# Kernel optimization log

Measured on AMD Instinct MI355X. Metric: run time of the kernel, lower is better.

Reference implementation:

```python
import jax, jax.numpy as jnp
import numpy as np

B = 4096
INPUT_SIZE = 256
OUT_WINDOW = 10
C = 16
OUTPUT_SIZE = 2  # real/imag pair
WIN = INPUT_SIZE - OUT_WINDOW + 1  # 247
BN_EPS = 1e-5


def setup_inputs() -> dict:
    key = jax.random.key(0)
    ks = jax.random.split(key, 7)
    return {
        "x": jax.random.normal(ks[0], (B, INPUT_SIZE, C, 2), dtype=jnp.float32),
        "W_in_real": jax.random.normal(ks[1], (C, WIN), dtype=jnp.float32),
        "W_in_imag": jax.random.normal(ks[2], (C, WIN), dtype=jnp.float32),
        "W_nl": jax.random.normal(ks[3], (C, OUTPUT_SIZE, 2 * (C - 1)), dtype=jnp.float32) * 0.1,
        "W_coeff": jax.random.normal(ks[4], (OUTPUT_SIZE, OUTPUT_SIZE), dtype=jnp.float32),
        "W_out_real": jax.random.normal(ks[5], (C, OUT_WINDOW), dtype=jnp.float32),
        "W_out_imag": jax.random.normal(ks[6], (C, OUT_WINDOW), dtype=jnp.float32),
        "bn_gamma": jnp.ones((C,), jnp.float32),
        "bn_beta": jnp.zeros((C,), jnp.float32),
    }


def _depthwise_filter(x_bcn, w_ck):
    # per-channel valid cross-correlation: out[b,c,w] = sum_k x[b,c,w+k] * w_ck[c,k]
    kern = w_ck[:, None, :]  # (O=C, I/groups=1, K)
    return jax.lax.conv_general_dilated(
        x_bcn, kern, window_strides=(1,), padding="VALID",
        dimension_numbers=("NCH", "OIH", "NCH"), feature_group_count=C)


def reference(x, W_in_real, W_in_imag, W_nl, W_coeff, W_out_real, W_out_imag, bn_gamma, bn_beta):
    # x: [B, N, C, 2]
    x_real = jnp.transpose(x[..., 0], (0, 2, 1))  # [B, C, N]
    x_imag = jnp.transpose(x[..., 1], (0, 2, 1))
    # unfold + per-channel FIR filter == depthwise valid correlation -> [B, W, C]
    f_r = jnp.transpose(_depthwise_filter(x_real, W_in_real), (0, 2, 1))
    f_i = jnp.transpose(_depthwise_filter(x_imag, W_in_imag), (0, 2, 1))
    # cubic amplitude nonlinearity
    amp = f_r * f_r + f_i * f_i
    f_r = amp * f_r
    f_i = amp * f_i
    # masked cross-channel gather (all channels except self), static indices
    nbr = np.stack([np.delete(np.arange(C), c) for c in range(C)])  # [C, C-1]
    nonlin_in = jnp.concatenate([f_r[:, :, nbr], f_i[:, :, nbr]], axis=-1)  # [B, W, C, 2(C-1)]
    # per-channel mixing then shared coeff mix
    nonlin_out = jnp.einsum("bwcf,cof->bwco", nonlin_in, W_nl)   # [B, W, C, 2]
    coeff_out = jnp.einsum("bwco,po->bwcp", nonlin_out, W_coeff)  # [B, W, C, 2]
    # per-channel output FIR over the out_window axis
    out_r = jnp.einsum("bwc,cw->bc", coeff_out[..., 0], W_out_real)
    out_i = jnp.einsum("bwc,cw->bc", coeff_out[..., 1], W_out_imag)
    out = jnp.stack([out_r, out_i], axis=-1)  # [B, C, 2]
    # BatchNorm1d over channel axis C (training mode, biased batch stats)
    mu = jnp.mean(out, axis=(0, 2))
    var = jnp.mean(jnp.square(out - mu[None, :, None]), axis=(0, 2))
    scale = (bn_gamma * jax.lax.rsqrt(var + BN_EPS))[None, :, None]
    return (out - mu[None, :, None]) * scale + bn_beta[None, :, None]
```

## Files before the change

### kernel.cpp

```cpp
#include <hip/hip_runtime.h>

#define BTOT 4096
#define G 4
#define NC 16
#define WIN 247
#define NBLK (BTOT / G)

typedef float v2f __attribute__((ext_vector_type(2)));

#define F2IDX(m, c) ((m) * 16 + (c) + ((m) >> 6) * 8)
#define WTSZ 4272

__global__ __launch_bounds__(256, 4) void k_main(
    const float* __restrict__ x,
    const float* __restrict__ Wr, const float* __restrict__ Wi,
    const float* __restrict__ Wnl, const float* __restrict__ Wc,
    const float* __restrict__ Wor, const float* __restrict__ Woi,
    float* __restrict__ out, float2* __restrict__ p2)
{
    __shared__ v2f WT[WTSZ];
    __shared__ float Mlds[4 * 16 * 17];
    __shared__ float WoS[2 * 160];
    __shared__ float WcS[4];

    const int tid  = threadIdx.x;
    const int lane = tid & 63;
    const int wv   = tid >> 6;
    const int jj   = lane >> 4;
    const int c    = lane & 15;
    const int b0   = blockIdx.x * G;

    for (int idx = tid; idx < 265 * 16; idx += 256) {
        int m = idx >> 4, cc = idx & 15;
        int t = m - 9;
        v2f v = (v2f)(0.f);
        if (t >= 0 && t < WIN) { v.x = Wr[cc * WIN + t]; v.y = Wi[cc * WIN + t]; }
        WT[F2IDX(m, cc)] = v;
    }
    for (int idx = tid; idx < 1024; idx += 256) {
        int m  = idx >> 8;
        int cc = (idx >> 4) & 15;
        int j  = idx & 15;
        float v = 0.f;
        if (j != cc) {
            int jp = j - (j > cc);
            v = Wnl[cc * 60 + (m >> 1) * 30 + (m & 1) * 15 + jp];
        }
        Mlds[m * 272 + cc * 17 + j] = v;
    }
    if (tid < 160) { WoS[tid] = Wor[tid]; WoS[160 + tid] = Woi[tid]; }
    if (tid < 4) WcS[tid] = Wc[tid];
    __syncthreads();

    const v2f* xq = (const v2f*)x + (size_t)(b0 + wv) * 4096 + lane;

    v2f acc[10];
    v2f win[14];
    v2f xr[8];
    #pragma unroll
    for (int w = 0; w < 10; ++w) acc[w] = (v2f)(0.f);

    #pragma unroll
    for (int d = 0; d < 14; ++d) win[d] = WT[F2IDX(d + jj, c)];
    #pragma unroll
    for (int j = 0; j < 8; ++j) xr[j] = xq[j * 64];

    #pragma unroll
    for (int i = 0; i < 64; ++i) {
        v2f xv = xr[i & 7];
        if (i < 56) xr[i & 7] = xq[(i + 8) * 64];
        #pragma unroll
        for (int w = 0; w < 10; ++w) {
            v2f wt = win[(i * 4 + 9 - w) % 14];
            acc[w] = __builtin_elementwise_fma(xv, wt, acc[w]);
        }
        #pragma unroll
        for (int d = 0; d < 4; ++d) {
            const int mb = i * 4 + 14 + d;
            if (mb <= 261) win[mb % 14] = WT[F2IDX(mb + jj, c)];
        }
    }

    #pragma unroll
    for (int w = 0; w < 10; ++w) {
        acc[w].x += __shfl_xor(acc[w].x, 16);  acc[w].x += __shfl_xor(acc[w].x, 32);
        acc[w].y += __shfl_xor(acc[w].y, 16);  acc[w].y += __shfl_xor(acc[w].y, 32);
    }

    __syncthreads();
    float* S    = (float*)WT;
    float* fbuf = S;
    float* crS  = S + 1280;
    float* ciS  = S + 1920;

    if (lane < 16) {
        #pragma unroll
        for (int w = 0; w < 10; ++w) {
            float fr = acc[w].x, fi = acc[w].y;
            float a  = fr * fr + fi * fi;
            fbuf[wv * 320 + c * 20 + w]      = a * fr;
            fbuf[wv * 320 + c * 20 + 10 + w] = a * fi;
        }
    }
    __syncthreads();

    const float* M0r = Mlds;
    const float* M0i = Mlds + 272;
    const float* M1r = Mlds + 544;
    const float* M1i = Mlds + 816;
    for (int idx = tid; idx < G * 160; idx += 256) {
        int bb = idx / 160; int r = idx - bb * 160;
        int cc = r / 10;    int w = r - cc * 10;
        const float* f3 = fbuf + bb * 320;
        float s0 = 0.f, s1 = 0.f;
        #pragma unroll
        for (int j = 0; j < NC; ++j) {
            float f3r = f3[j * 20 + w];
            float f3i = f3[j * 20 + 10 + w];
            s0 = fmaf(f3r, M0r[cc * 17 + j], fmaf(f3i, M0i[cc * 17 + j], s0));
            s1 = fmaf(f3r, M1r[cc * 17 + j], fmaf(f3i, M1i[cc * 17 + j], s1));
        }
        float p0 = s0 * WcS[0] + s1 * WcS[1];
        float p1 = s0 * WcS[2] + s1 * WcS[3];
        crS[idx] = p0 * WoS[cc * 10 + w];
        ciS[idx] = p1 * WoS[160 + cc * 10 + w];
    }
    __syncthreads();

    if (tid < G * NC) {
        int bb = tid >> 4; int cc = tid & 15;
        float orr = 0.f, oii = 0.f;
        #pragma unroll
        for (int w = 0; w < 10; ++w) {
            orr += crS[bb * 160 + cc * 10 + w];
            oii += ciS[bb * 160 + cc * 10 + w];
        }
        size_t o = ((size_t)(b0 + bb) * NC + cc) * 2;
        out[o]     = orr;
        out[o + 1] = oii;
        float s1 = orr + oii;
        float q1 = orr * orr + oii * oii;
        s1 += __shfl_xor(s1, 16);  s1 += __shfl_xor(s1, 32);
        q1 += __shfl_xor(q1, 16);  q1 += __shfl_xor(q1, 32);
        if (tid < NC)
            p2[tid * NBLK + blockIdx.x] = make_float2(s1, q1);
    }
}

__global__ __launch_bounds__(256) void k_bn(
    const float2* __restrict__ p2,
    const float* __restrict__ gamma, const float* __restrict__ beta,
    float* __restrict__ out)
{
    __shared__ float A[16], Bb[16];
    const int tid = threadIdx.x;
    const int cch = tid >> 4;
    const int t   = tid & 15;

    float s = 0.f, q = 0.f;
    #pragma unroll 8
    for (int k = 0; k < NBLK / 16; ++k) {
        float2 v = p2[cch * NBLK + t + 16 * k];
        s += v.x; q += v.y;
    }
    #pragma unroll
    for (int off = 1; off < 16; off <<= 1) {
        s += __shfl_xor(s, off);
        q += __shfl_xor(q, off);
    }
    if (t == 0) {
        const float inv_n = 1.f / (BTOT * 2.f);
        float mu  = s * inv_n;
        float var = q * inv_n - mu * mu;
        float sc  = gamma[cch] * rsqrtf(var + 1e-5f);
        A[cch]  = sc;
        Bb[cch] = beta[cch] - mu * sc;
    }
    __syncthreads();

    float4* o4 = (float4*)out;
    const int base = blockIdx.x * 512;
    #pragma unroll
    for (int i = 0; i < 2; ++i) {
        int f = base + i * 256 + tid;
        float4 v = o4[f];
        int cp = (f & 7) * 2;
        v.x = v.x * A[cp]     + Bb[cp];
        v.y = v.y * A[cp]     + Bb[cp];
        v.z = v.z * A[cp + 1] + Bb[cp + 1];
        v.w = v.w * A[cp + 1] + Bb[cp + 1];
        o4[f] = v;
    }
}

extern "C" void kernel_launch(void* const* d_in, const int* in_sizes, int n_in,
                              void* d_out, int out_size, void* d_ws, size_t ws_size,
                              hipStream_t stream)
{
    const float* x    = (const float*)d_in[0];
    const float* Wr   = (const float*)d_in[1];
    const float* Wi   = (const float*)d_in[2];
    const float* Wnl  = (const float*)d_in[3];
    const float* Wc   = (const float*)d_in[4];
    const float* Wor  = (const float*)d_in[5];
    const float* Woi  = (const float*)d_in[6];
    const float* gam  = (const float*)d_in[7];
    const float* bet  = (const float*)d_in[8];
    float* out = (float*)d_out;
    float2* p2 = (float2*)d_ws;

    k_main<<<NBLK, 256, 0, stream>>>(x, Wr, Wi, Wnl, Wc, Wor, Woi, out, p2);
    k_bn<<<64, 256, 0, stream>>>(p2, gam, bet, out);
}
```

Baseline: 43.49 us.

## Stage input through LDS with float4 loads and double blocks per CTA

Each wave now reads its batch row with coalesced float4 global loads into a per-wave LDS ring buffer, and the convolution consumes the v2f values from LDS. The weight window grows to 16 registers so ring indexing becomes a mask instead of a modulo. Block size doubles to 512 threads covering 8 batches, which halves the number of weight-table staging passes, and the partial BN statistics layout is adjusted to match. This adds LDS traffic and per-wave LDS footprint, and the wider per-thread loads may raise register pressure.

New measurement: 61.17 us. 1.41x slower.

```diff
diff --git a/kernel.cpp b/kernel.cpp
--- a/kernel.cpp
+++ b/kernel.cpp
@@ -1,7 +1,7 @@
 #include <hip/hip_runtime.h>
 
 #define BTOT 4096
-#define G 4
+#define G 8
 #define NC 16
 #define WIN 247
 #define NBLK (BTOT / G)
@@ -11,7 +11,22 @@
 #define F2IDX(m, c) ((m) * 16 + (c) + ((m) >> 6) * 8)
 #define WTSZ 4272
 
-__global__ __launch_bounds__(256, 4) void k_main(
+#define CONV_STEP(TT, SS, GUARDED)                                                       \
+    {                                                                                    \
+        v2f xv = xlv[((TT) & 3) * 128 + ((SS) * 4 + jj) * 16 + c];                       \
+        _Pragma("unroll")                                                                \
+        for (int w = 0; w < 10; ++w)                                                     \
+            acc[w] = __builtin_elementwise_fma(                                          \
+                xv, win[((2 * (TT) + (SS)) * 4 + 9 - w) & 15], acc[w]);                  \
+        _Pragma("unroll")                                                                \
+        for (int d = 0; d < 4; ++d) {                                                    \
+            const int mb = (2 * (TT) + (SS)) * 4 + 16 + d;                               \
+            if (!(GUARDED) || mb <= 261)                                                 \
+                win[((2 * (TT) + (SS)) * 4 + d) & 15] = WT[F2IDX(mb + jj, c)];           \
+        }                                                                                \
+    }
+
+__global__ __launch_bounds__(512, 4) void k_main(
     const float* __restrict__ x,
     const float* __restrict__ Wr, const float* __restrict__ Wi,
     const float* __restrict__ Wnl, const float* __restrict__ Wc,
@@ -19,6 +34,7 @@
     float* __restrict__ out, float2* __restrict__ p2)
 {
     __shared__ v2f WT[WTSZ];
+    __shared__ float4 XL[G][4][64];
     __shared__ float Mlds[4 * 16 * 17];
     __shared__ float WoS[2 * 160];
     __shared__ float WcS[4];
@@ -30,14 +46,14 @@
     const int c    = lane & 15;
     const int b0   = blockIdx.x * G;
 
-    for (int idx = tid; idx < 265 * 16; idx += 256) {
+    for (int idx = tid; idx < 265 * 16; idx += 512) {
         int m = idx >> 4, cc = idx & 15;
         int t = m - 9;
         v2f v = (v2f)(0.f);
         if (t >= 0 && t < WIN) { v.x = Wr[cc * WIN + t]; v.y = Wi[cc * WIN + t]; }
         WT[F2IDX(m, cc)] = v;
     }
-    for (int idx = tid; idx < 1024; idx += 256) {
+    for (int idx = tid; idx < 1024; idx += 512) {
         int m  = idx >> 8;
         int cc = (idx >> 4) & 15;
         int j  = idx & 15;
@@ -52,34 +68,40 @@
     if (tid < 4) WcS[tid] = Wc[tid];
     __syncthreads();
 
-    const v2f* xq = (const v2f*)x + (size_t)(b0 + wv) * 4096 + lane;
+    const float4* gx = (const float4*)(x + (size_t)(b0 + wv) * 8192);
+    v2f* xlv = (v2f*)&XL[wv][0][0];
 
     v2f acc[10];
-    v2f win[14];
-    v2f xr[8];
+    v2f win[16];
+    float4 chq[4];
     #pragma unroll
     for (int w = 0; w < 10; ++w) acc[w] = (v2f)(0.f);
-
-    #pragma unroll
-    for (int d = 0; d < 14; ++d) win[d] = WT[F2IDX(d + jj, c)];
-    #pragma unroll
-    for (int j = 0; j < 8; ++j) xr[j] = xq[j * 64];
-
-    #pragma unroll
-    for (int i = 0; i < 64; ++i) {
-        v2f xv = xr[i & 7];
-        if (i < 56) xr[i & 7] = xq[(i + 8) * 64];
-        #pragma unroll
-        for (int w = 0; w < 10; ++w) {
-            v2f wt = win[(i * 4 + 9 - w) % 14];
-            acc[w] = __builtin_elementwise_fma(xv, wt, acc[w]);
-        }
-        #pragma unroll
-        for (int d = 0; d < 4; ++d) {
-            const int mb = i * 4 + 14 + d;
-            if (mb <= 261) win[mb % 14] = WT[F2IDX(mb + jj, c)];
-        }
-    }
+    #pragma unroll
+    for (int d = 0; d < 16; ++d) win[d] = WT[F2IDX(d + jj, c)];
+
+    chq[0] = gx[lane];
+    chq[1] = gx[64 + lane];
+    chq[2] = gx[128 + lane];
+    chq[3] = gx[192 + lane];
+    XL[wv][0][lane] = chq[0];
+
+    for (int tq = 0; tq < 7; ++tq) {
+        #pragma unroll
+        for (int k = 0; k < 4; ++k) {
+            const int t = tq * 4 + k;
+            chq[k] = gx[(t + 4) * 64 + lane];
+            XL[wv][(k + 1) & 3][lane] = chq[(k + 1) & 3];
+            CONV_STEP(t, 0, 0)
+            CONV_STEP(t, 1, 0)
+        }
+    }
+    XL[wv][1][lane] = chq[1];
+    CONV_STEP(28, 0, 1) CONV_STEP(28, 1, 1)
+    XL[wv][2][lane] = chq[2];
+    CONV_STEP(29, 0, 1) CONV_STEP(29, 1, 1)
+    XL[wv][3][lane] = chq[3];
+    CONV_STEP(30, 0, 1) CONV_STEP(30, 1, 1)
+    CONV_STEP(31, 0, 1) CONV_STEP(31, 1, 1)
 
     #pragma unroll
     for (int w = 0; w < 10; ++w) {
@@ -90,8 +112,8 @@
     __syncthreads();
     float* S    = (float*)WT;
     float* fbuf = S;
-    float* crS  = S + 1280;
-    float* ciS  = S + 1920;
+    float* crS  = S + 2560;
+    float* ciS  = S + 3840;
 
     if (lane < 16) {
         #pragma unroll
@@ -108,7 +130,7 @@
     const float* M0i = Mlds + 272;
     const float* M1r = Mlds + 544;
     const float* M1i = Mlds + 816;
-    for (int idx = tid; idx < G * 160; idx += 256) {
+    for (int idx = tid; idx < G * 160; idx += 512) {
         int bb = idx / 160; int r = idx - bb * 160;
         int cc = r / 10;    int w = r - cc * 10;
         const float* f3 = fbuf + bb * 320;
@@ -142,8 +164,8 @@
         float q1 = orr * orr + oii * oii;
         s1 += __shfl_xor(s1, 16);  s1 += __shfl_xor(s1, 32);
         q1 += __shfl_xor(q1, 16);  q1 += __shfl_xor(q1, 32);
-        if (tid < NC)
-            p2[tid * NBLK + blockIdx.x] = make_float2(s1, q1);
+        if ((tid & 63) < 16)
+            p2[cc * (2 * NBLK) + blockIdx.x * 2 + (tid >> 6)] = make_float2(s1, q1);
     }
 }
 
@@ -159,8 +181,8 @@
 
     float s = 0.f, q = 0.f;
     #pragma unroll 8
-    for (int k = 0; k < NBLK / 16; ++k) {
-        float2 v = p2[cch * NBLK + t + 16 * k];
+    for (int k = 0; k < (2 * NBLK) / 16; ++k) {
+        float2 v = p2[cch * (2 * NBLK) + t + 16 * k];
         s += v.x; q += v.y;
     }
     #pragma unroll
@@ -209,6 +231,6 @@
     float* out = (float*)d_out;
     float2* p2 = (float2*)d_ws;
 
-    k_main<<<NBLK, 256, 0, stream>>>(x, Wr, Wi, Wnl, Wc, Wor, Woi, out, p2);
+    k_main<<<NBLK, 512, 0, stream>>>(x, Wr, Wi, Wnl, Wc, Wor, Woi, out, p2);
     k_bn<<<64, 256, 0, stream>>>(p2, gam, bet, out);
 }
```
